# Kernel optimization log

Measured on AMD Instinct MI355X. Metric: run time of the kernel, lower is better.

Reference implementation:

```python
import jax, jax.numpy as jnp
import numpy as np

GAIN_RELU = float(np.sqrt(2.0))  # torch.nn.init.calculate_gain('relu')
EPS = 1e-12  # F.normalize eps

N_NODES = 50000
N_EDGES = 1600000
IN_DIM = 8
HID = 32
EMB = 32


def setup_inputs() -> dict:
    key = jax.random.key(0)
    ks = jax.random.split(key, 20)
    x = jax.random.normal(ks[0], (N_NODES, IN_DIM), dtype=jnp.float32)
    edge_index = jax.random.randint(ks[1], (2, N_EDGES), 0, N_NODES, dtype=jnp.int64)
    d = {"x": x, "edge_index": edge_index}
    # Three WeBConv layers: (in->HID), (3*HID->HID), (3*HID->EMB)
    dims = [(IN_DIM, HID), (3 * HID, HID), (3 * HID, EMB)]
    ki = 2
    for li, (din, dout) in enumerate(dims, start=1):
        s = 1.0 / np.sqrt(din)  # torch Linear default init scale (uniform)
        d[f"w{li}_up"] = jax.random.uniform(ks[ki], (dout, din), jnp.float32, -s, s); ki += 1
        d[f"w{li}_down"] = jax.random.uniform(ks[ki], (dout, din), jnp.float32, -s, s); ki += 1
        d[f"w{li}_bias"] = jax.random.uniform(ks[ki], (dout, din), jnp.float32, -s, s); ki += 1
        d[f"ew{li}_up"] = jax.random.normal(ks[ki], (N_EDGES,), jnp.float32) * GAIN_RELU; ki += 1
        d[f"ew{li}_down"] = jax.random.normal(ks[ki], (N_EDGES,), jnp.float32) * GAIN_RELU; ki += 1
    return d


def _propagate(xp, src, dst, edge_weight, n_nodes):
    # degree-normalized (1/deg of target), edge-weighted scatter-add
    deg = jnp.zeros((n_nodes,), xp.dtype).at[dst].add(1.0)
    deg_inv = jnp.where(deg > 0, 1.0 / deg, 0.0)  # inf -> 0
    w = deg_inv[dst] * edge_weight  # [E]
    msgs = w[:, None] * xp[src]  # [E, F] gather + scale
    return jnp.zeros((n_nodes, xp.shape[1]), xp.dtype).at[dst].add(msgs)


def _webconv(x, edge_index, w_up, w_down, w_bias, ew_up, ew_down):
    n = x.shape[0]
    row, col = edge_index[0], edge_index[1]
    up_x = x @ w_up.T
    down_x = x @ w_down.T
    bias_x = x @ w_bias.T
    x_up = _propagate(up_x, row, col, ew_up, n)          # normal direction
    x_down = _propagate(down_x, col, row, ew_down, n)    # flipud(edge_index)
    cat = jnp.concatenate([x_up, x_down, bias_x], axis=-1)
    norm = jnp.maximum(jnp.linalg.norm(cat, axis=-1, keepdims=True), EPS)
    return cat / norm


def reference(x, edge_index,
              w1_up, w1_down, w1_bias, ew1_up, ew1_down,
              w2_up, w2_down, w2_bias, ew2_up, ew2_down,
              w3_up, w3_down, w3_bias, ew3_up, ew3_down):
    act = lambda h: jax.nn.leaky_relu(h, negative_slope=0.1)
    h = act(_webconv(x, edge_index, w1_up, w1_down, w1_bias, ew1_up, ew1_down))
    h = act(_webconv(h, edge_index, w2_up, w2_down, w2_bias, ew2_up, ew2_down))
    h = act(_webconv(h, edge_index, w3_up, w3_down, w3_bias, ew3_up, ew3_down))
    mean_up = (ew1_up + ew2_up + ew3_up) / 3.0
    mean_down = (ew1_down + ew2_down + ew3_down) / 3.0
    return h, mean_up, mean_down
```

## Files before the change

kernel.cpp:

```cpp
#include <hip/hip_runtime.h>
#include <hip/hip_bf16.h>
#include <math.h>

typedef __hip_bfloat16 bf16;
typedef unsigned short ushort_t;
typedef unsigned int uint_t;
typedef __attribute__((ext_vector_type(8))) short bf16x8;
typedef __attribute__((ext_vector_type(4))) float f32x4;

#define NBMAX 1024
#define BSH 8
#define CH 2560
#define NCMAX 2048
#define CSRCAP 6144

__device__ __forceinline__ float ldf(const void* p, long i, int isbf) {
    return isbf ? __bfloat162float(((const bf16*)p)[i]) : ((const float*)p)[i];
}
__device__ __forceinline__ int lde(const int* ei, int half, long e, long E, int is64) {
    long idx = half ? (E + e) : e;
    if (is64) return ((const int2*)ei)[idx].x;
    return ei[idx];
}
__device__ __forceinline__ float u2f(ushort_t u) {
    union { unsigned int i; float f; } v; v.i = ((unsigned)u) << 16; return v.f;
}
__device__ __forceinline__ ushort_t f2u(float f) {
    bf16 h = __float2bfloat16(f);
    return *reinterpret_cast<ushort_t*>(&h);
}
__device__ __forceinline__ float lo2f(unsigned sp) {
    union { unsigned i; float f; } v; v.i = sp << 16; return v.f;
}
__device__ __forceinline__ float hi2f(unsigned sp) {
    union { unsigned i; float f; } v; v.i = sp & 0xffff0000u; return v.f;
}

struct DetectArgs {
    const void* p[16];
    long n[16];
    const int* ei;
    long E;
    int* flags;
};

__global__ void k_detect(DetectArgs a) {
    __shared__ int cnt;
    if (threadIdx.x == 0) cnt = 0;
    __syncthreads();
    int b = blockIdx.x;
    int bad = 0;
    if (b < 16) {
        const bf16* p = (const bf16*)a.p[b];
        long m = a.n[b] < 4096 ? a.n[b] : 4096;
        for (long i = threadIdx.x; i < m; i += 256) {
            float v = __bfloat162float(p[i]);
            if (!(fabsf(v) < 100.0f)) bad++;
        }
        atomicAdd(&cnt, bad);
        __syncthreads();
        if (threadIdx.x == 0) a.flags[b] = ((long)cnt * 16 < m) ? 1 : 0;
    } else {
        long m = a.E / 2 < 4096 ? a.E / 2 : 4096;
        for (long i = threadIdx.x; i < m; i += 256) {
            if (a.ei[2 * i + 1] != 0) bad++;
        }
        atomicAdd(&cnt, bad);
        __syncthreads();
        if (threadIdx.x == 0) a.flags[16] = (cnt < (int)(m / 16) + 1) ? 1 : 0;
    }
}


__global__ void kb_count(const int* __restrict__ ei, long E, const int* __restrict__ flags,
                         int NB, int NC, int* __restrict__ hc) {
    __shared__ int h0[NBMAX], h1[NBMAX];
    for (int i = threadIdx.x; i < NB; i += 256) { h0[i] = 0; h1[i] = 0; }
    __syncthreads();
    int is64 = flags[16];
    int c = blockIdx.x;
    long base = (long)c * CH;
#pragma unroll
    for (int i = 0; i < CH / 256; i++) {
        long e = base + i * 256 + threadIdx.x;
        if (e < E) {
            int cc = lde(ei, 1, e, E, is64);
            int rr = lde(ei, 0, e, E, is64);
            atomicAdd(&h0[cc >> BSH], 1);
            atomicAdd(&h1[rr >> BSH], 1);
        }
    }
    __syncthreads();
    for (int b = threadIdx.x; b < NB; b += 256) {
        hc[((long)0 * NC + c) * NB + b] = h0[b];
        hc[((long)1 * NC + c) * NB + b] = h1[b];
    }
}

__global__ void kb_scanA(int* __restrict__ hc, int NC, int NB, int* __restrict__ bc) {
    __shared__ int ssum[256];
    int b = blockIdx.x, d = blockIdx.y;
    int tid = threadIdx.x;
    int k = (NC + 255) / 256;
    int c0 = tid * k;
    int local[8];
    int s = 0;
    for (int i = 0; i < k; i++) {
        int c = c0 + i;
        int v = (c < NC) ? hc[((long)d * NC + c) * NB + b] : 0;
        local[i] = s; s += v;
    }
    ssum[tid] = s;
    __syncthreads();
    for (int dd = 1; dd < 256; dd <<= 1) {
        int t = (tid >= dd) ? ssum[tid - dd] : 0;
        __syncthreads();
        ssum[tid] += t;
        __syncthreads();
    }
    int base = ssum[tid] - s;
    for (int i = 0; i < k; i++) {
        int c = c0 + i;
        if (c < NC) hc[((long)d * NC + c) * NB + b] = base + local[i];
    }
    if (tid == 255) bc[d * NBMAX + b] = ssum[255];
}

__global__ void kb_scanB(const int* __restrict__ bc, int* __restrict__ bb, int NB) {
    if (threadIdx.x < 2) {
        int dir = threadIdx.x;
        int acc = 0;
        for (int i = 0; i < NB; i++) { bb[dir * (NBMAX + 1) + i] = acc; acc += bc[dir * NBMAX + i]; }
        bb[dir * (NBMAX + 1) + NB] = acc;
    }
}

__global__ __launch_bounds__(512) void kb_fill(
                        const int* __restrict__ ei, long E, const int* __restrict__ flags,
                        int NB, int NBp, int NC,
                        const int* __restrict__ hc, const int* __restrict__ bb,
                        const void* __restrict__ eu1, const void* __restrict__ eu2,
                        const void* __restrict__ eu3, const void* __restrict__ ed1,
                        const void* __restrict__ ed2, const void* __restrict__ ed3,
                        int2* __restrict__ bse_a, ushort_t* __restrict__ bse_w3) {
    extern __shared__ char dynlds[];
    int2* ssA      = (int2*)dynlds;
    ushort_t* ssW  = (ushort_t*)(ssA + CH);
    ushort_t* sbkt = ssW + CH;
    int* h    = (int*)(sbkt + CH);
    int* lofs = h + NBp;
    int* cur  = lofs + NBp;
    int* gb   = cur + NBp;
    int tid = threadIdx.x;
    int cidx = blockIdx.x;
    int dir = blockIdx.y;
    int is64 = flags[16];
    const void* w1p = dir ? ed1 : eu1;
    const void* w2p = dir ? ed2 : eu2;
    const void* w3p = dir ? ed3 : eu3;
    int f1 = flags[dir ? 5 : 4], f2 = flags[dir ? 10 : 9], f3 = flags[dir ? 15 : 14];
    for (int i = tid; i < NBp; i += 512) { h[i] = 0; cur[i] = 0; }
    for (int b = tid; b < NB; b += 512)
        gb[b] = bb[dir * (NBMAX + 1) + b] + hc[((long)dir * NC + cidx) * NB + b];
    __syncthreads();
    long base = (long)cidx * CH;
    const int EPT = CH / 512;
    int myd[EPT], mys[EPT], myw12[EPT];
    ushort_t myw3[EPT];
#pragma unroll
    for (int i = 0; i < EPT; i++) {
        long e = base + i * 512 + tid;
        myd[i] = -1;
        if (e < E) {
            myd[i] = lde(ei, dir ? 0 : 1, e, E, is64);
            mys[i] = lde(ei, dir ? 1 : 0, e, E, is64);
            myw12[i] = (unsigned)f2u(ldf(w1p, e, f1)) | ((unsigned)f2u(ldf(w2p, e, f2)) << 16);
            myw3[i] = f2u(ldf(w3p, e, f3));
            atomicAdd(&h[myd[i] >> BSH], 1);
        }
    }
    __syncthreads();
    if (tid < 64) {
        int carry = 0;
        for (int g = 0; g < NBp; g += 64) {
            int idx = g + tid;
            int v = (idx < NBp) ? h[idx] : 0;
            int x = v;
#pragma unroll
            for (int o = 1; o < 64; o <<= 1) {
                int y = __shfl_up(x, o, 64);
                if (tid >= o) x += y;
            }
            if (idx < NBp) lofs[idx] = x - v + carry;
            carry += __shfl(x, 63, 64);
        }
    }
    __syncthreads();
#pragma unroll
    for (int i = 0; i < EPT; i++) {
        if (myd[i] >= 0) {
            int b = myd[i] >> BSH;
            int r = atomicAdd(&cur[b], 1);
            int p = lofs[b] + r;
            ssA[p] = make_int2(mys[i] | ((myd[i] & 255) << 24), myw12[i]);
            ssW[p] = myw3[i];
            sbkt[p] = (ushort_t)b;
        }
    }
    __syncthreads();
    long rem = E - base;
    int nvalid = rem >= CH ? CH : (rem > 0 ? (int)rem : 0);
    int2* osA = bse_a + (long)dir * E;
    ushort_t* osW = bse_w3 + (long)dir * E;
    for (int s = tid; s < nvalid; s += 512) {
        int b = sbkt[s];
        long p = (long)gb[b] + (s - lofs[b]);
        osA[p] = ssA[s];
        osW[p] = ssW[s];
    }
}

__global__ __launch_bounds__(512) void kb_csr(
                       const int* __restrict__ bb, const int2* __restrict__ bse_a,
                       const ushort_t* __restrict__ bse_w3,
                       long E, int NB, long N,
                       int* __restrict__ off_c, int* __restrict__ off_r,
                       int* __restrict__ list_c, int* __restrict__ list_r,
                       ushort_t* __restrict__ wc6) {
    __shared__ int2 sA[CSRCAP];
    __shared__ ushort_t sW[CSRCAP];
    __shared__ int h[256], lofs[256], cur[256];
    int tid = threadIdx.x;
    int b = blockIdx.x, dir = blockIdx.y;
    int base = bb[dir * (NBMAX + 1) + b];
    int cnt  = bb[dir * (NBMAX + 1) + b + 1] - base;
    const int2* bsA = bse_a + (long)dir * E;
    const ushort_t* bsW = bse_w3 + (long)dir * E;
    int* off  = dir ? off_r : off_c;
    int* list = dir ? list_r : list_c;
    ushort_t* o1 = wc6 + (long)(0 + dir) * E;
    ushort_t* o2 = wc6 + (long)(2 + dir) * E;
    ushort_t* o3 = wc6 + (long)(4 + dir) * E;
    if (tid < 256) { h[tid] = 0; cur[tid] = 0; }
    __syncthreads();
    int nb0 = b << BSH;
    for (int s = tid; s < cnt; s += 512)
        atomicAdd(&h[(unsigned)bsA[base + s].x >> 24], 1);
    __syncthreads();
    if (tid < 64) {
        int carry = 0;
#pragma unroll
        for (int g = 0; g < 4; g++) {
            int idx = g * 64 + tid;
            int v = h[idx];
            int x = v;
#pragma unroll
            for (int o = 1; o < 64; o <<= 1) {
                int y = __shfl_up(x, o, 64);
                if (tid >= o) x += y;
            }
            lofs[idx] = x - v + carry;
            carry += __shfl(x, 63, 64);
        }
    }
    __syncthreads();
    if (tid < 256) {
        long n = (long)nb0 + tid;
        if (n < N) off[n] = base + lofs[tid];
    }
    if (b == 0 && tid == 0) off[N] = (int)E;
    int mid = lofs[128];
    int cnt1 = cnt - mid;
    if (mid <= CSRCAP && cnt1 <= CSRCAP) {
        for (int s = tid; s < cnt; s += 512) {
            int2 se = bsA[base + s];
            int local = (unsigned)se.x >> 24;
            if (local < 128) {
                int r = atomicAdd(&cur[local], 1);
                int p = lofs[local] + r;
                sA[p] = se;
                sW[p] = bsW[base + s];
            }
        }
        __syncthreads();
        for (int s = tid; s < mid; s += 512) {
            int2 se = sA[s];
            list[base + s] = se.x & 0xFFFFFF;
            o1[base + s] = (ushort_t)((unsigned)se.y & 0xFFFF);
            o2[base + s] = (ushort_t)((unsigned)se.y >> 16);
            o3[base + s] = sW[s];
        }
        __syncthreads();
        for (int s = tid; s < cnt; s += 512) {
            int2 se = bsA[base + s];
            int local = (unsigned)se.x >> 24;
            if (local >= 128) {
                int r = atomicAdd(&cur[local], 1);
                int p = lofs[local] - mid + r;
                sA[p] = se;
                sW[p] = bsW[base + s];
            }
        }
        __syncthreads();
        for (int s = tid; s < cnt1; s += 512) {
            int2 se = sA[s];
            list[base + mid + s] = se.x & 0xFFFFFF;
            o1[base + mid + s] = (ushort_t)((unsigned)se.y & 0xFFFF);
            o2[base + mid + s] = (ushort_t)((unsigned)se.y >> 16);
            o3[base + mid + s] = sW[s];
        }
    } else {
        for (int s = tid; s < cnt; s += 512) {
            int2 se = bsA[base + s];
            int local = (unsigned)se.x >> 24;
            int r = atomicAdd(&cur[local], 1);
            long p = (long)base + lofs[local] + r;
            list[p] = se.x & 0xFFFFFF;
            o1[p] = (ushort_t)((unsigned)se.y & 0xFFFF);
            o2[p] = (ushort_t)((unsigned)se.y >> 16);
            o3[p] = bsW[base + s];
        }
    }
}

__device__ __forceinline__ void gedge1(const int* __restrict__ list, const ushort_t* __restrict__ wc,
                                       const ushort_t* __restrict__ S, int j, int f4,
                                       float& a0, float& a1, float& a2, float& a3) {
    int s0 = list[j];
    float w0 = u2f(wc[j]);
    uint2 p0 = *(const uint2*)&S[((long)s0 << 5) + (f4 << 2)];
    a0 += w0 * lo2f(p0.x);
    a1 += w0 * hi2f(p0.x);
    a2 += w0 * lo2f(p0.y);
    a3 += w0 * hi2f(p0.y);
}
__device__ __forceinline__ void gacc4(const int* __restrict__ list, const ushort_t* __restrict__ wc,
                                      const ushort_t* __restrict__ S, int j0, int j1, int sub, int f4,
                                      float& a0, float& a1, float& a2, float& a3) {
    int deg = j1 - j0;
    int len = (deg + 3) >> 2;
    int j = j0 + sub * len;
    int je = j + len; if (je > j1) je = j1;
    if (j < je && (j & 1)) { gedge1(list, wc, S, j, f4, a0, a1, a2, a3); j++; }
    for (; j + 3 < je; j += 4) {
        int2 s01 = *(const int2*)&list[j];
        int2 s23 = *(const int2*)&list[j + 2];
        uint_t w01 = *(const uint_t*)&wc[j];
        uint_t w23 = *(const uint_t*)&wc[j + 2];
        uint2 p0 = *(const uint2*)&S[((long)s01.x << 5) + (f4 << 2)];
        uint2 p1 = *(const uint2*)&S[((long)s01.y << 5) + (f4 << 2)];
        uint2 p2 = *(const uint2*)&S[((long)s23.x << 5) + (f4 << 2)];
        uint2 p3 = *(const uint2*)&S[((long)s23.y << 5) + (f4 << 2)];
        float w0 = lo2f(w01), w1 = hi2f(w01), w2 = lo2f(w23), w3 = hi2f(w23);
        a0 += w0 * lo2f(p0.x) + w1 * lo2f(p1.x) + w2 * lo2f(p2.x) + w3 * lo2f(p3.x);
        a1 += w0 * hi2f(p0.x) + w1 * hi2f(p1.x) + w2 * hi2f(p2.x) + w3 * hi2f(p3.x);
        a2 += w0 * lo2f(p0.y) + w1 * lo2f(p1.y) + w2 * lo2f(p2.y) + w3 * lo2f(p3.y);
        a3 += w0 * hi2f(p0.y) + w1 * hi2f(p1.y) + w2 * hi2f(p2.y) + w3 * hi2f(p3.y);
    }
    if (j + 1 < je) {
        int2 s01 = *(const int2*)&list[j];
        uint_t w01 = *(const uint_t*)&wc[j];
        uint2 p0 = *(const uint2*)&S[((long)s01.x << 5) + (f4 << 2)];
        uint2 p1 = *(const uint2*)&S[((long)s01.y << 5) + (f4 << 2)];
        float w0 = lo2f(w01), w1 = hi2f(w01);
        a0 += w0 * lo2f(p0.x) + w1 * lo2f(p1.x);
        a1 += w0 * hi2f(p0.x) + w1 * hi2f(p1.x);
        a2 += w0 * lo2f(p0.y) + w1 * lo2f(p1.y);
        a3 += w0 * hi2f(p0.y) + w1 * hi2f(p1.y);
        j += 2;
    }
    if (j < je) gedge1(list, wc, S, j, f4, a0, a1, a2, a3);
}

__global__ void k_gather_up(const int* __restrict__ off_c, const int* __restrict__ list_c,
                            const ushort_t* __restrict__ wcu, const ushort_t* __restrict__ Su,
                            long N, float* __restrict__ U) {
    long t = (long)blockIdx.x * blockDim.x + threadIdx.x;
    long pair = t >> 6;
    int lane = (int)(t & 63);
    long n = pair * 2 + (lane >> 5);
    if (n >= N) return;
    int hl = lane & 31;
    int sub = hl >> 3;
    int f4  = hl & 7;
    int j0 = off_c[n], j1 = off_c[n + 1];
    float a0 = 0.f, a1 = 0.f, a2 = 0.f, a3 = 0.f;
    gacc4(list_c, wcu, Su, j0, j1, sub, f4, a0, a1, a2, a3);
    a0 += __shfl_xor(a0, 8, 32);  a1 += __shfl_xor(a1, 8, 32);
    a2 += __shfl_xor(a2, 8, 32);  a3 += __shfl_xor(a3, 8, 32);
    a0 += __shfl_xor(a0, 16, 32); a1 += __shfl_xor(a1, 16, 32);
    a2 += __shfl_xor(a2, 16, 32); a3 += __shfl_xor(a3, 16, 32);
    if (sub == 0) {
        int deg = j1 - j0;
        float dinv = (deg > 0) ? 1.0f / (float)deg : 0.f;
        *(float4*)&U[(n << 5) + (f4 << 2)] =
            make_float4(a0 * dinv, a1 * dinv, a2 * dinv, a3 * dinv);
    }
}

__global__ void k_gather_downfin(const int* __restrict__ off_r, const int* __restrict__ list_r,
                                 const ushort_t* __restrict__ wcd, const ushort_t* __restrict__ Sd,
                                 const ushort_t* __restrict__ Sb, const float* __restrict__ U,
                                 long N, float* __restrict__ out) {
    long t = (long)blockIdx.x * blockDim.x + threadIdx.x;
    long pair = t >> 6;
    int lane = (int)(t & 63);
    long n = pair * 2 + (lane >> 5);
    if (n >= N) return;
    int hl = lane & 31;
    int sub = hl >> 3;
    int f4  = hl & 7;
    int j0 = off_r[n], j1 = off_r[n + 1];
    float a0 = 0.f, a1 = 0.f, a2 = 0.f, a3 = 0.f;
    gacc4(list_r, wcd, Sd, j0, j1, sub, f4, a0, a1, a2, a3);
    a0 += __shfl_xor(a0, 8, 32);  a1 += __shfl_xor(a1, 8, 32);
    a2 += __shfl_xor(a2, 8, 32);  a3 += __shfl_xor(a3, 8, 32);
    a0 += __shfl_xor(a0, 16, 32); a1 += __shfl_xor(a1, 16, 32);
    a2 += __shfl_xor(a2, 16, 32); a3 += __shfl_xor(a3, 16, 32);
    float v0 = 0.f, v1 = 0.f, v2 = 0.f, v3 = 0.f;
    float u0 = 0.f, u1 = 0.f, u2 = 0.f, u3 = 0.f;
    float c0 = 0.f, c1 = 0.f, c2 = 0.f, c3 = 0.f;
    float ss = 0.f;
    if (sub == 0) {
        int deg = j1 - j0;
        float dinv = (deg > 0) ? 1.0f / (float)deg : 0.f;
        v0 = a0 * dinv; v1 = a1 * dinv; v2 = a2 * dinv; v3 = a3 * dinv;
        float4 uv = *(const float4*)&U[(n << 5) + (f4 << 2)];
        u0 = uv.x; u1 = uv.y; u2 = uv.z; u3 = uv.w;
        uint2 bp = *(const uint2*)&Sb[(n << 5) + (f4 << 2)];
        c0 = lo2f(bp.x); c1 = hi2f(bp.x); c2 = lo2f(bp.y); c3 = hi2f(bp.y);
        ss = v0 * v0 + v1 * v1 + v2 * v2 + v3 * v3
           + u0 * u0 + u1 * u1 + u2 * u2 + u3 * u3
           + c0 * c0 + c1 * c1 + c2 * c2 + c3 * c3;
    }
#pragma unroll
    for (int m = 1; m < 32; m <<= 1) ss += __shfl_xor(ss, m, 32);
    float inv = 1.0f / fmaxf(sqrtf(ss), 1e-12f);
    if (sub == 0) {
        float x0, x1, x2, x3;
        x0 = u0 * inv; x0 = (x0 >= 0.f) ? x0 : 0.1f * x0;
        x1 = u1 * inv; x1 = (x1 >= 0.f) ? x1 : 0.1f * x1;
        x2 = u2 * inv; x2 = (x2 >= 0.f) ? x2 : 0.1f * x2;
        x3 = u3 * inv; x3 = (x3 >= 0.f) ? x3 : 0.1f * x3;
        *(float4*)&out[n * 96 + (f4 << 2)] = make_float4(x0, x1, x2, x3);
        x0 = v0 * inv; x0 = (x0 >= 0.f) ? x0 : 0.1f * x0;
        x1 = v1 * inv; x1 = (x1 >= 0.f) ? x1 : 0.1f * x1;
        x2 = v2 * inv; x2 = (x2 >= 0.f) ? x2 : 0.1f * x2;
        x3 = v3 * inv; x3 = (x3 >= 0.f) ? x3 : 0.1f * x3;
        *(float4*)&out[n * 96 + 32 + (f4 << 2)] = make_float4(x0, x1, x2, x3);
        x0 = c0 * inv; x0 = (x0 >= 0.f) ? x0 : 0.1f * x0;
        x1 = c1 * inv; x1 = (x1 >= 0.f) ? x1 : 0.1f * x1;
        x2 = c2 * inv; x2 = (x2 >= 0.f) ? x2 : 0.1f * x2;
        x3 = c3 * inv; x3 = (x3 >= 0.f) ? x3 : 0.1f * x3;
        *(float4*)&out[n * 96 + 64 + (f4 << 2)] = make_float4(x0, x1, x2, x3);
    }
}

__global__ __launch_bounds__(256) void k_lin96(
                        const float* __restrict__ xin, long N,
                        const void* __restrict__ wu, const void* __restrict__ wd,
                        const void* __restrict__ wb, int wfi,
                        const int* __restrict__ flags,
                        ushort_t* __restrict__ Su, ushort_t* __restrict__ Sd,
                        ushort_t* __restrict__ Sb) {
    __shared__ ushort_t wlds[6 * 3 * 64 * 8];
    __shared__ ushort_t alds[64 * 104];
    int tid = threadIdx.x;
    int ubf = flags[wfi], dbf = flags[wfi + 1], bbf = flags[wfi + 2];
    for (int idx = tid; idx < 6 * 3 * 64; idx += 256) {
        int t = idx / (3 * 64);
        int rem = idx - t * 3 * 64;
        int s = rem >> 6;
        int l = rem & 63;
        int n = t * 16 + (l & 15);
        int kg = l >> 4;
        const void* w = (n < 32) ? wu : (n < 64) ? wd : wb;
        int f = (n < 32) ? ubf : (n < 64) ? dbf : bbf;
        int o = n & 31;
        ushort_t tmp[8];
#pragma unroll
        for (int j = 0; j < 8; j++)
            tmp[j] = f2u(ldf(w, (long)o * 96 + s * 32 + kg * 8 + j, f));
        *(bf16x8*)&wlds[idx * 8] = *(const bf16x8*)tmp;
    }
    long nb = (long)blockIdx.x * 64;
    for (int j = tid; j < 64 * 24; j += 256) {
        int node = j / 24, c = j % 24;
        long gn = nb + node;
        float4 v = make_float4(0.f, 0.f, 0.f, 0.f);
        if (gn < N) v = ((const float4*)(xin + gn * 96))[c];
        ushort_t* dst = &alds[node * 104 + c * 4];
        dst[0] = f2u(v.x); dst[1] = f2u(v.y); dst[2] = f2u(v.z); dst[3] = f2u(v.w);
    }
    __syncthreads();
    int wv = tid >> 6;
    int lane = tid & 63;
    int m0 = lane & 15;
    int kg = lane >> 4;
    int row = wv * 16 + m0;
    f32x4 acc[6];
#pragma unroll
    for (int t = 0; t < 6; t++) acc[t] = (f32x4){0.f, 0.f, 0.f, 0.f};
#pragma unroll
    for (int s = 0; s < 3; s++) {
        bf16x8 a = *(const bf16x8*)&alds[row * 104 + s * 32 + kg * 8];
#pragma unroll
        for (int t = 0; t < 6; t++) {
            bf16x8 b = *(const bf16x8*)&wlds[((t * 3 + s) * 64 + lane) * 8];
            acc[t] = __builtin_amdgcn_mfma_f32_16x16x32_bf16(a, b, acc[t], 0, 0, 0);
        }
    }
    __syncthreads();
    ushort_t* sbuf = alds;
#pragma unroll
    for (int t = 0; t < 6; t++) {
        int n = t * 16 + (lane & 15);
#pragma unroll
        for (int r = 0; r < 4; r++) {
            int m = (lane >> 4) * 4 + r;
            sbuf[(wv * 16 + m) * 96 + n] = f2u(acc[t][r]);
        }
    }
    __syncthreads();
    for (int j = tid; j < 64 * 96; j += 256) {
        int nd = j / 96, o3 = j % 96;
        long gn = nb + nd;
        if (gn < N) {
            int blk = o3 >> 5, fo = o3 & 31;
            ushort_t v = sbuf[j];
            (blk == 0 ? Su : blk == 1 ? Sd : Sb)[gn * 32 + fo] = v;
        }
    }
}

__global__ void k_linear_b16(const void* __restrict__ xin, int xfi, int din, int dout, long N,
                             const void* __restrict__ wu, const void* __restrict__ wd,
                             const void* __restrict__ wb, int wfi,
                             const int* __restrict__ flags, int uselds,
                             ushort_t* __restrict__ Su, ushort_t* __restrict__ Sd,
                             ushort_t* __restrict__ Sb) {
    __shared__ float smem[12288];
    int xbf = (xfi >= 0) ? flags[xfi] : 0;
    int ubf = flags[wfi], dbf = flags[wfi + 1], bbf = flags[wfi + 2];
    float* su = smem;
    float* sd = smem + (long)din * dout;
    float* sb = smem + 2l * din * dout;
    if (uselds) {
        for (int j = threadIdx.x; j < din * dout; j += 256) {
            int o = j % dout, i = j / dout;
            su[j] = ldf(wu, (long)o * din + i, ubf);
            sd[j] = ldf(wd, (long)o * din + i, dbf);
            sb[j] = ldf(wb, (long)o * din + i, bbf);
        }
        __syncthreads();
    }
    long idx = (long)blockIdx.x * blockDim.x + threadIdx.x;
    long node = idx / dout;
    int o = (int)(idx % dout);
    if (node >= N) return;
    float au = 0.f, ad = 0.f, ab = 0.f;
    long xb = node * din;
    if (uselds) {
        for (int i = 0; i < din; i++) {
            float xv = ldf(xin, xb + i, xbf);
            au += xv * su[i * dout + o];
            ad += xv * sd[i * dout + o];
            ab += xv * sb[i * dout + o];
        }
    } else {
        for (int i = 0; i < din; i++) {
            float xv = ldf(xin, xb + i, xbf);
            au += xv * ldf(wu, (long)o * din + i, ubf);
            ad += xv * ldf(wd, (long)o * din + i, dbf);
            ab += xv * ldf(wb, (long)o * din + i, bbf);
        }
    }
    Su[node * dout + o] = f2u(au);
    Sd[node * dout + o] = f2u(ad);
    Sb[node * dout + o] = f2u(ab);
}

__global__ void k_linear(const void* __restrict__ xin, int xfi, int din, int dout, int rs, long N,
                         const void* __restrict__ wu, const void* __restrict__ wd,
                         const void* __restrict__ wb, int wfi,
                         const int* __restrict__ flags, int uselds,
                         float* __restrict__ A, float* __restrict__ B, float* __restrict__ C) {
    __shared__ float smem[12288];
    int xbf = (xfi >= 0) ? flags[xfi] : 0;
    int ubf = flags[wfi], dbf = flags[wfi + 1], bbf = flags[wfi + 2];
    float* su = smem;
    float* sd = smem + (long)din * dout;
    float* sb = smem + 2l * din * dout;
    if (uselds) {
        for (int j = threadIdx.x; j < din * dout; j += 256) {
            int o = j % dout, i = j / dout;
            su[j] = ldf(wu, (long)o * din + i, ubf);
            sd[j] = ldf(wd, (long)o * din + i, dbf);
            sb[j] = ldf(wb, (long)o * din + i, bbf);
        }
        __syncthreads();
    }
    long idx = (long)blockIdx.x * blockDim.x + threadIdx.x;
    long node = idx / dout;
    int o = (int)(idx % dout);
    if (node >= N) return;
    float au = 0.f, ad = 0.f, ab = 0.f;
    long xb = node * din;
    if (uselds) {
        for (int i = 0; i < din; i++) {
            float xv = ldf(xin, xb + i, xbf);
            au += xv * su[i * dout + o];
            ad += xv * sd[i * dout + o];
            ab += xv * sb[i * dout + o];
        }
    } else {
        for (int i = 0; i < din; i++) {
            float xv = ldf(xin, xb + i, xbf);
            au += xv * ldf(wu, (long)o * din + i, ubf);
            ad += xv * ldf(wd, (long)o * din + i, dbf);
            ab += xv * ldf(wb, (long)o * din + i, bbf);
        }
    }
    A[node * rs + o] = au;
    B[node * rs + o] = ad;
    C[node * rs + o] = ab;
}

__global__ void k_deg(const int* __restrict__ ei, long E, const int* __restrict__ flags,
                      float* __restrict__ degc, float* __restrict__ degr) {
    long e = (long)blockIdx.x * blockDim.x + threadIdx.x;
    if (e < E) {
        int is64 = flags[16];
        atomicAdd(&degc[lde(ei, 1, e, E, is64)], 1.0f);
        atomicAdd(&degr[lde(ei, 0, e, E, is64)], 1.0f);
    }
}

__global__ void k_inv(float* __restrict__ a, long n) {
    long i = (long)blockIdx.x * blockDim.x + threadIdx.x;
    if (i < n) { float v = a[i]; a[i] = (v > 0.0f) ? 1.0f / v : 0.0f; }
}

__global__ void k_scatter(const int* __restrict__ ei, long E, int F,
                          const void* __restrict__ ewu, const void* __restrict__ ewd,
                          int fu, int fd, const int* __restrict__ flags,
                          const float* __restrict__ degci, const float* __restrict__ degri,
                          const float* __restrict__ A, const float* __restrict__ B,
                          float* __restrict__ U, float* __restrict__ D) {
    long idx = (long)blockIdx.x * blockDim.x + threadIdx.x;
    long tot = E * 2 * F;
    if (idx >= tot) return;
    int is64 = flags[16];
    long e = idx / (2 * F);
    int rem = (int)(idx - e * 2 * F);
    int dir = rem >= F;
    int f = rem - dir * F;
    int r = lde(ei, 0, e, E, is64), c = lde(ei, 1, e, E, is64);
    if (!dir) {
        float w = degci[c] * ldf(ewu, e, flags[fu]);
        atomicAdd(&U[(long)c * F + f], w * A[(long)r * F + f]);
    } else {
        float w = degri[r] * ldf(ewd, e, flags[fd]);
        atomicAdd(&D[(long)r * F + f], w * B[(long)c * F + f]);
    }
}

__global__ void k_finalize(const float* __restrict__ U, const float* __restrict__ D,
                           const float* __restrict__ C, int F, long N,
                           float* __restrict__ out) {
    long t = (long)blockIdx.x * blockDim.x + threadIdx.x;
    long n = t >> 6;
    if (n >= N) return;
    int lane = (int)(t & 63);
    int cat = 3 * F;
    float ss = 0.f;
    for (int j = lane; j < cat; j += 64) {
        float v = (j < F) ? U[n * F + j] : (j < 2 * F) ? D[n * F + j - F] : C[n * F + j - 2 * F];
        ss += v * v;
    }
#pragma unroll
    for (int m = 1; m < 64; m <<= 1) ss += __shfl_xor(ss, m, 64);
    float inv = 1.0f / fmaxf(sqrtf(ss), 1e-12f);
    for (int j = lane; j < cat; j += 64) {
        float v = (j < F) ? U[n * F + j] : (j < 2 * F) ? D[n * F + j - F] : C[n * F + j - 2 * F];
        float a = v * inv;
        a = (a >= 0.0f) ? a : 0.1f * a;
        out[n * cat + j] = a;
    }
}

__global__ void k_mean(const void* e1u, const void* e2u, const void* e3u,
                       const void* e1d, const void* e2d, const void* e3d,
                       const int* __restrict__ flags, long E,
                       float* __restrict__ mu, float* __restrict__ md) {
    long e = (long)blockIdx.x * blockDim.x + threadIdx.x;
    if (e >= E) return;
    float su = ldf(e1u, e, flags[4]) + ldf(e2u, e, flags[9]) + ldf(e3u, e, flags[14]);
    float sd = ldf(e1d, e, flags[5]) + ldf(e2d, e, flags[10]) + ldf(e3d, e, flags[15]);
    mu[e] = su / 3.0f;
    md[e] = sd / 3.0f;
}

extern "C" void kernel_launch(void* const* d_in, const int* in_sizes, int n_in,
                              void* d_out, int out_size, void* d_ws, size_t ws_size,
                              hipStream_t stream) {
    const int* ei = (const int*)d_in[1];
    const void* w_up[3]   = {d_in[2], d_in[7],  d_in[12]};
    const void* w_down[3] = {d_in[3], d_in[8],  d_in[13]};
    const void* w_bias[3] = {d_in[4], d_in[9],  d_in[14]};
    const void* ew_up[3]  = {d_in[5], d_in[10], d_in[15]};
    const void* ew_down[3]= {d_in[6], d_in[11], d_in[16]};

    long E = in_sizes[5];
    if (E <= 0) E = 1600000;
    int HID = (int)(sqrt((double)in_sizes[7] / 3.0) + 0.5);
    if (HID <= 0 || (long)3 * HID * HID != (long)in_sizes[7]) HID = 32;
    int DIN = in_sizes[2] / HID;
    if (DIN <= 0) DIN = 8;
    long N = (long)in_sizes[0] / DIN;
    if (N <= 0) N = 50000;
    int EMB = in_sizes[12] / (3 * HID);
    if (EMB <= 0) EMB = 32;
    int Fm = HID > EMB ? HID : EMB;
    int NB = (int)((N + 255) >> BSH);
    int NBp = (NB + 1) & ~1;
    int NC = (int)((E + CH - 1) / CH);

    float* out_h  = (float*)d_out;
    float* out_mu = out_h + N * 3l * EMB;
    float* out_md = out_mu + E;

    const int TB = 256;
    int lds1  = (3l * DIN * HID <= 12288) ? 1 : 0;
    int lds12 = (3l * (3 * HID) * HID <= 12288) ? 1 : 0;
    int lds3  = (3l * (3 * HID) * EMB <= 12288) ? 1 : 0;
    dim3 linG1((unsigned)((N * HID + TB - 1) / TB));
    dim3 linG3((unsigned)((N * EMB + TB - 1) / TB));
    dim3 lin96G((unsigned)((N + 63) / 64));
    dim3 finG((unsigned)((N * 64 + TB - 1) / TB));
    long npair = (N + 1) / 2;
    dim3 finG2((unsigned)((npair * 64 + TB - 1) / TB));
    dim3 edgeG((unsigned)((E + TB - 1) / TB));
    dim3 chunkG1((unsigned)NC);
    dim3 chunkG2((unsigned)NC, 2);
    size_t fillLds = (size_t)CH * 12 + (size_t)(4 * NBp) * 4;

    int* flags = (int*)d_ws;
    int* bc    = flags + 64;
    int* bb    = bc + 2 * NBMAX;
    int* off_c = bb + 2 * (NBMAX + 1);
    int* off_r = off_c + (N + 1);
    int* hc    = off_r + (N + 1);
    long li = (long)(hc + 2l * NC * NB - (int*)d_ws);
    li = (li + 3) & ~3l;
    int* list_c = (int*)d_ws + li;
    int* list_r = list_c + E;
    ushort_t* wc6 = (ushort_t*)(list_r + E);
    int* X = list_r + E + 3 * E;
    int2* bse_a = (int2*)X;
    ushort_t* bse_w3 = (ushort_t*)(X + 4 * E);
    ushort_t* Su = (ushort_t*)X;
    ushort_t* Sd = Su + N * Fm;
    ushort_t* Sb = Sd + N * Fm;
    float* U = (float*)(Sb + N * Fm);
    long zInts = (3l * N * Fm + 1) / 2 + N * Fm;
    long Xints = 5l * E;
    if (zInts > Xints) Xints = zInts;
    size_t need = (size_t)((li + 5l * E + Xints) * 4l + 256);

    bool fast = (HID == 32 && EMB == 32) && (NB <= NBMAX) && (NC <= NCMAX) &&
                (ws_size == 0 || ws_size >= need);

    DetectArgs da;
    da.p[0] = d_in[0]; da.n[0] = in_sizes[0];
    for (int L = 0; L < 3; L++) {
        da.p[1 + 5 * L] = w_up[L];    da.n[1 + 5 * L] = in_sizes[2 + 5 * L];
        da.p[2 + 5 * L] = w_down[L];  da.n[2 + 5 * L] = in_sizes[3 + 5 * L];
        da.p[3 + 5 * L] = w_bias[L];  da.n[3 + 5 * L] = in_sizes[4 + 5 * L];
        da.p[4 + 5 * L] = ew_up[L];   da.n[4 + 5 * L] = in_sizes[5 + 5 * L];
        da.p[5 + 5 * L] = ew_down[L]; da.n[5 + 5 * L] = in_sizes[6 + 5 * L];
    }
    da.ei = ei; da.E = E; da.flags = flags;
    k_detect<<<17, TB, 0, stream>>>(da);

    if (fast) {
        kb_count<<<chunkG1, TB, 0, stream>>>(ei, E, flags, NB, NC, hc);
        kb_scanA<<<dim3((unsigned)NB, 2), 256, 0, stream>>>(hc, NC, NB, bc);
        kb_scanB<<<1, 64, 0, stream>>>(bc, bb, NB);
        kb_fill<<<chunkG2, 512, fillLds, stream>>>(ei, E, flags, NB, NBp, NC, hc, bb,
                                                   ew_up[0], ew_up[1], ew_up[2],
                                                   ew_down[0], ew_down[1], ew_down[2],
                                                   bse_a, bse_w3);
        kb_csr<<<dim3((unsigned)NB, 2), 512, 0, stream>>>(bb, bse_a, bse_w3, E, NB, N,
                                                          off_c, off_r, list_c, list_r,
                                                          wc6);

        k_mean<<<edgeG, TB, 0, stream>>>(ew_up[0], ew_up[1], ew_up[2],
                                         ew_down[0], ew_down[1], ew_down[2],
                                         flags, E, out_mu, out_md);

        float* H = (float*)d_out;

        k_linear_b16<<<linG1, TB, 0, stream>>>(d_in[0], 0, DIN, HID, N,
                                               w_up[0], w_down[0], w_bias[0], 1, flags, lds1,
                                               Su, Sd, Sb);
        k_gather_up<<<finG2, TB, 0, stream>>>(off_c, list_c, wc6, Su, N, U);
        k_gather_downfin<<<finG2, TB, 0, stream>>>(off_r, list_r, wc6 + E, Sd, Sb, U, N, H);
        k_lin96<<<lin96G, 256, 0, stream>>>(H, N, w_up[1], w_down[1], w_bias[1], 6, flags,
                                            Su, Sd, Sb);
        k_gather_up<<<finG2, TB, 0, stream>>>(off_c, list_c, wc6 + 2l * E, Su, N, U);
        k_gather_downfin<<<finG2, TB, 0, stream>>>(off_r, list_r, wc6 + 3l * E, Sd, Sb, U, N, H);
        k_lin96<<<lin96G, 256, 0, stream>>>(H, N, w_up[2], w_down[2], w_bias[2], 11, flags,
                                            Su, Sd, Sb);
        k_gather_up<<<finG2, TB, 0, stream>>>(off_c, list_c, wc6 + 4l * E, Su, N, U);
        k_gather_downfin<<<finG2, TB, 0, stream>>>(off_r, list_r, wc6 + 5l * E, Sd, Sb, U, N, out_h);
    } else {
        float* degci = (float*)(flags + 64);
        float* degri = degci + N;
        float* fA = degri + N;
        float* fB = fA + N * Fm;
        float* fC = fB + N * Fm;
        float* fU = fC + N * Fm;
        float* fD = fU + N * Fm;
        float* fH = fD + N * Fm;
        dim3 scatG12((unsigned)((E * 2 * HID + TB - 1) / TB));
        dim3 scatG3((unsigned)((E * 2 * EMB + TB - 1) / TB));

        hipMemsetAsync(degci, 0, 2 * N * sizeof(float), stream);
        k_deg<<<edgeG, TB, 0, stream>>>(ei, E, flags, degci, degri);
        k_inv<<<dim3((unsigned)((2 * N + TB - 1) / TB)), TB, 0, stream>>>(degci, 2 * N);

        k_linear<<<linG1, TB, 0, stream>>>(d_in[0], 0, DIN, HID, HID, N,
                                           w_up[0], w_down[0], w_bias[0], 1, flags, lds1, fA, fB, fC);
        hipMemsetAsync(fU, 0, 2l * N * Fm * sizeof(float), stream);
        k_scatter<<<scatG12, TB, 0, stream>>>(ei, E, HID, ew_up[0], ew_down[0], 4, 5, flags,
                                              degci, degri, fA, fB, fU, fD);
        k_finalize<<<finG, TB, 0, stream>>>(fU, fD, fC, HID, N, fH);

        k_linear<<<linG1, TB, 0, stream>>>(fH, -1, 3 * HID, HID, HID, N,
                                           w_up[1], w_down[1], w_bias[1], 6, flags, lds12, fA, fB, fC);
        hipMemsetAsync(fU, 0, 2l * N * Fm * sizeof(float), stream);
        k_scatter<<<scatG12, TB, 0, stream>>>(ei, E, HID, ew_up[1], ew_down[1], 9, 10, flags,
                                              degci, degri, fA, fB, fU, fD);
        k_finalize<<<finG, TB, 0, stream>>>(fU, fD, fC, HID, N, fH);

        k_linear<<<linG3, TB, 0, stream>>>(fH, -1, 3 * HID, EMB, EMB, N,
                                           w_up[2], w_down[2], w_bias[2], 11, flags, lds3, fA, fB, fC);
        hipMemsetAsync(fU, 0, 2l * N * Fm * sizeof(float), stream);
        k_scatter<<<scatG3, TB, 0, stream>>>(ei, E, EMB, ew_up[2], ew_down[2], 14, 15, flags,
                                             degci, degri, fA, fB, fU, fD);
        k_finalize<<<finG, TB, 0, stream>>>(fU, fD, fC, EMB, N, out_h);

        k_mean<<<edgeG, TB, 0, stream>>>(ew_up[0], ew_up[1], ew_up[2],
                                         ew_down[0], ew_down[1], ew_down[2],
                                         flags, E, out_mu, out_md);
    }
}
```

Before: 456.7 us.

## Fuse up and down gathers into one kernel, one node per wavefront

Replaces the separate up-gather and down-gather-plus-finalize kernels with a single kernel. Each 64-lane wavefront handles one node: the lower half gathers along the column CSR, the upper half along the row CSR, and the L2 norm is reduced across the full wave. This removes the intermediate fp32 U buffer round-trip and one launch per layer. In exchange, each wave now mixes two neighbor lists of different length, so lanes may diverge and load imbalance can rise.

```diff
diff --git a/kernel.cpp b/kernel.cpp
--- a/kernel.cpp
+++ b/kernel.cpp
@@ -372,87 +372,61 @@
     if (j < je) gedge1(list, wc, S, j, f4, a0, a1, a2, a3);
 }
 
-__global__ void k_gather_up(const int* __restrict__ off_c, const int* __restrict__ list_c,
-                            const ushort_t* __restrict__ wcu, const ushort_t* __restrict__ Su,
-                            long N, float* __restrict__ U) {
+__global__ void k_gather_fused(const int* __restrict__ off_c, const int* __restrict__ list_c,
+                               const ushort_t* __restrict__ wcu, const ushort_t* __restrict__ Su,
+                               const int* __restrict__ off_r, const int* __restrict__ list_r,
+                               const ushort_t* __restrict__ wcd, const ushort_t* __restrict__ Sd,
+                               const ushort_t* __restrict__ Sb, long N,
+                               float* __restrict__ out) {
     long t = (long)blockIdx.x * blockDim.x + threadIdx.x;
-    long pair = t >> 6;
+    long n = t >> 6;
+    if (n >= N) return;
     int lane = (int)(t & 63);
-    long n = pair * 2 + (lane >> 5);
-    if (n >= N) return;
+    int half = lane >> 5;
     int hl = lane & 31;
     int sub = hl >> 3;
     int f4  = hl & 7;
-    int j0 = off_c[n], j1 = off_c[n + 1];
+    const int* off = half ? off_r : off_c;
+    const int* list = half ? list_r : list_c;
+    const ushort_t* wc = half ? wcd : wcu;
+    const ushort_t* S = half ? Sd : Su;
+    int j0 = off[n], j1 = off[n + 1];
     float a0 = 0.f, a1 = 0.f, a2 = 0.f, a3 = 0.f;
-    gacc4(list_c, wcu, Su, j0, j1, sub, f4, a0, a1, a2, a3);
+    gacc4(list, wc, S, j0, j1, sub, f4, a0, a1, a2, a3);
     a0 += __shfl_xor(a0, 8, 32);  a1 += __shfl_xor(a1, 8, 32);
     a2 += __shfl_xor(a2, 8, 32);  a3 += __shfl_xor(a3, 8, 32);
     a0 += __shfl_xor(a0, 16, 32); a1 += __shfl_xor(a1, 16, 32);
     a2 += __shfl_xor(a2, 16, 32); a3 += __shfl_xor(a3, 16, 32);
-    if (sub == 0) {
-        int deg = j1 - j0;
-        float dinv = (deg > 0) ? 1.0f / (float)deg : 0.f;
-        *(float4*)&U[(n << 5) + (f4 << 2)] =
-            make_float4(a0 * dinv, a1 * dinv, a2 * dinv, a3 * dinv);
-    }
-}
-
-__global__ void k_gather_downfin(const int* __restrict__ off_r, const int* __restrict__ list_r,
-                                 const ushort_t* __restrict__ wcd, const ushort_t* __restrict__ Sd,
-                                 const ushort_t* __restrict__ Sb, const float* __restrict__ U,
-                                 long N, float* __restrict__ out) {
-    long t = (long)blockIdx.x * blockDim.x + threadIdx.x;
-    long pair = t >> 6;
-    int lane = (int)(t & 63);
-    long n = pair * 2 + (lane >> 5);
-    if (n >= N) return;
-    int hl = lane & 31;
-    int sub = hl >> 3;
-    int f4  = hl & 7;
-    int j0 = off_r[n], j1 = off_r[n + 1];
-    float a0 = 0.f, a1 = 0.f, a2 = 0.f, a3 = 0.f;
-    gacc4(list_r, wcd, Sd, j0, j1, sub, f4, a0, a1, a2, a3);
-    a0 += __shfl_xor(a0, 8, 32);  a1 += __shfl_xor(a1, 8, 32);
-    a2 += __shfl_xor(a2, 8, 32);  a3 += __shfl_xor(a3, 8, 32);
-    a0 += __shfl_xor(a0, 16, 32); a1 += __shfl_xor(a1, 16, 32);
-    a2 += __shfl_xor(a2, 16, 32); a3 += __shfl_xor(a3, 16, 32);
-    float v0 = 0.f, v1 = 0.f, v2 = 0.f, v3 = 0.f;
-    float u0 = 0.f, u1 = 0.f, u2 = 0.f, u3 = 0.f;
+    int deg = j1 - j0;
+    float dinv = (deg > 0) ? 1.0f / (float)deg : 0.f;
+    float r0 = a0 * dinv, r1 = a1 * dinv, r2 = a2 * dinv, r3 = a3 * dinv;
     float c0 = 0.f, c1 = 0.f, c2 = 0.f, c3 = 0.f;
     float ss = 0.f;
     if (sub == 0) {
-        int deg = j1 - j0;
-        float dinv = (deg > 0) ? 1.0f / (float)deg : 0.f;
-        v0 = a0 * dinv; v1 = a1 * dinv; v2 = a2 * dinv; v3 = a3 * dinv;
-        float4 uv = *(const float4*)&U[(n << 5) + (f4 << 2)];
-        u0 = uv.x; u1 = uv.y; u2 = uv.z; u3 = uv.w;
-        uint2 bp = *(const uint2*)&Sb[(n << 5) + (f4 << 2)];
-        c0 = lo2f(bp.x); c1 = hi2f(bp.x); c2 = lo2f(bp.y); c3 = hi2f(bp.y);
-        ss = v0 * v0 + v1 * v1 + v2 * v2 + v3 * v3
-           + u0 * u0 + u1 * u1 + u2 * u2 + u3 * u3
-           + c0 * c0 + c1 * c1 + c2 * c2 + c3 * c3;
-    }
-#pragma unroll
-    for (int m = 1; m < 32; m <<= 1) ss += __shfl_xor(ss, m, 32);
+        ss = r0 * r0 + r1 * r1 + r2 * r2 + r3 * r3;
+        if (half == 0) {
+            uint2 bp = *(const uint2*)&Sb[(n << 5) + (f4 << 2)];
+            c0 = lo2f(bp.x); c1 = hi2f(bp.x); c2 = lo2f(bp.y); c3 = hi2f(bp.y);
+            ss += c0 * c0 + c1 * c1 + c2 * c2 + c3 * c3;
+        }
+    }
+#pragma unroll
+    for (int m = 1; m < 64; m <<= 1) ss += __shfl_xor(ss, m, 64);
     float inv = 1.0f / fmaxf(sqrtf(ss), 1e-12f);
     if (sub == 0) {
         float x0, x1, x2, x3;
-        x0 = u0 * inv; x0 = (x0 >= 0.f) ? x0 : 0.1f * x0;
-        x1 = u1 * inv; x1 = (x1 >= 0.f) ? x1 : 0.1f * x1;
-        x2 = u2 * inv; x2 = (x2 >= 0.f) ? x2 : 0.1f * x2;
-        x3 = u3 * inv; x3 = (x3 >= 0.f) ? x3 : 0.1f * x3;
-        *(float4*)&out[n * 96 + (f4 << 2)] = make_float4(x0, x1, x2, x3);
-        x0 = v0 * inv; x0 = (x0 >= 0.f) ? x0 : 0.1f * x0;
-        x1 = v1 * inv; x1 = (x1 >= 0.f) ? x1 : 0.1f * x1;
-        x2 = v2 * inv; x2 = (x2 >= 0.f) ? x2 : 0.1f * x2;
-        x3 = v3 * inv; x3 = (x3 >= 0.f) ? x3 : 0.1f * x3;
-        *(float4*)&out[n * 96 + 32 + (f4 << 2)] = make_float4(x0, x1, x2, x3);
-        x0 = c0 * inv; x0 = (x0 >= 0.f) ? x0 : 0.1f * x0;
-        x1 = c1 * inv; x1 = (x1 >= 0.f) ? x1 : 0.1f * x1;
-        x2 = c2 * inv; x2 = (x2 >= 0.f) ? x2 : 0.1f * x2;
-        x3 = c3 * inv; x3 = (x3 >= 0.f) ? x3 : 0.1f * x3;
-        *(float4*)&out[n * 96 + 64 + (f4 << 2)] = make_float4(x0, x1, x2, x3);
+        x0 = r0 * inv; x0 = (x0 >= 0.f) ? x0 : 0.1f * x0;
+        x1 = r1 * inv; x1 = (x1 >= 0.f) ? x1 : 0.1f * x1;
+        x2 = r2 * inv; x2 = (x2 >= 0.f) ? x2 : 0.1f * x2;
+        x3 = r3 * inv; x3 = (x3 >= 0.f) ? x3 : 0.1f * x3;
+        *(float4*)&out[n * 96 + half * 32 + (f4 << 2)] = make_float4(x0, x1, x2, x3);
+        if (half == 0) {
+            x0 = c0 * inv; x0 = (x0 >= 0.f) ? x0 : 0.1f * x0;
+            x1 = c1 * inv; x1 = (x1 >= 0.f) ? x1 : 0.1f * x1;
+            x2 = c2 * inv; x2 = (x2 >= 0.f) ? x2 : 0.1f * x2;
+            x3 = c3 * inv; x3 = (x3 >= 0.f) ? x3 : 0.1f * x3;
+            *(float4*)&out[n * 96 + 64 + (f4 << 2)] = make_float4(x0, x1, x2, x3);
+        }
     }
 }
 
@@ -738,8 +712,6 @@
     dim3 linG3((unsigned)((N * EMB + TB - 1) / TB));
     dim3 lin96G((unsigned)((N + 63) / 64));
     dim3 finG((unsigned)((N * 64 + TB - 1) / TB));
-    long npair = (N + 1) / 2;
-    dim3 finG2((unsigned)((npair * 64 + TB - 1) / TB));
     dim3 edgeG((unsigned)((E + TB - 1) / TB));
     dim3 chunkG1((unsigned)NC);
     dim3 chunkG2((unsigned)NC, 2);
@@ -762,7 +734,6 @@
     ushort_t* Su = (ushort_t*)X;
     ushort_t* Sd = Su + N * Fm;
     ushort_t* Sb = Sd + N * Fm;
-    float* U = (float*)(Sb + N * Fm);
     long zInts = (3l * N * Fm + 1) / 2 + N * Fm;
     long Xints = 5l * E;
     if (zInts > Xints) Xints = zInts;
@@ -804,16 +775,16 @@
         k_linear_b16<<<linG1, TB, 0, stream>>>(d_in[0], 0, DIN, HID, N,
                                                w_up[0], w_down[0], w_bias[0], 1, flags, lds1,
                                                Su, Sd, Sb);
-        k_gather_up<<<finG2, TB, 0, stream>>>(off_c, list_c, wc6, Su, N, U);
-        k_gather_downfin<<<finG2, TB, 0, stream>>>(off_r, list_r, wc6 + E, Sd, Sb, U, N, H);
+        k_gather_fused<<<finG, TB, 0, stream>>>(off_c, list_c, wc6, Su,
+                                                off_r, list_r, wc6 + E, Sd, Sb, N, H);
         k_lin96<<<lin96G, 256, 0, stream>>>(H, N, w_up[1], w_down[1], w_bias[1], 6, flags,
                                             Su, Sd, Sb);
-        k_gather_up<<<finG2, TB, 0, stream>>>(off_c, list_c, wc6 + 2l * E, Su, N, U);
-        k_gather_downfin<<<finG2, TB, 0, stream>>>(off_r, list_r, wc6 + 3l * E, Sd, Sb, U, N, H);
+        k_gather_fused<<<finG, TB, 0, stream>>>(off_c, list_c, wc6 + 2l * E, Su,
+                                                off_r, list_r, wc6 + 3l * E, Sd, Sb, N, H);
         k_lin96<<<lin96G, 256, 0, stream>>>(H, N, w_up[2], w_down[2], w_bias[2], 11, flags,
                                             Su, Sd, Sb);
-        k_gather_up<<<finG2, TB, 0, stream>>>(off_c, list_c, wc6 + 4l * E, Su, N, U);
-        k_gather_downfin<<<finG2, TB, 0, stream>>>(off_r, list_r, wc6 + 5l * E, Sd, Sb, U, N, out_h);
+        k_gather_fused<<<finG, TB, 0, stream>>>(off_c, list_c, wc6 + 4l * E, Su,
+                                                off_r, list_r, wc6 + 5l * E, Sd, Sb, N, out_h);
     } else {
         float* degci = (float*)(flags + 64);
         float* degri = degci + N;
```

Measured after the change: 474.1 us. +3.8%, slower.
